# Performance work log

Hardware: AMD Instinct MI355X
Metric: run time of the kernel (lower is better)

Reference implementation:

```python
import jax, jax.numpy as jnp
import numpy as np

N = 50000      # nodes
E = 800000     # edges
D = 128        # node_feat_dim
ED = 64        # edge_feat_dim
C = 10         # num_fine_classes
BN_EPS = 1e-5


def _lin(key, fan_in, fan_out):
    k1, k2 = jax.random.split(key)
    s = 1.0 / np.sqrt(fan_in)
    W = jax.random.uniform(k1, (fan_in, fan_out), jnp.float32, -s, s)
    b = jax.random.uniform(k2, (fan_out,), jnp.float32, -s, s)
    return W, b


def setup_inputs() -> dict:
    key = jax.random.key(0)
    ks = jax.random.split(key, 16)
    nfeats = jax.random.normal(ks[0], (N, D), jnp.float32)
    efeats = jax.random.normal(ks[1], (E, ED), jnp.float32)
    src = jax.random.randint(ks[2], (E,), 0, N, jnp.int64 if jax.config.jax_enable_x64 else jnp.int32)
    dst = jax.random.randint(ks[3], (E,), 0, N, src.dtype)
    # SAGE layer 1 and 2 (E-GraphSAGE style)
    Wm1, bm1 = _lin(ks[4], D + ED, D)   # W_msg: cat(h_src, e) -> D
    Wa1, ba1 = _lin(ks[5], 2 * D, D)    # W_apply: cat(h, h_neigh) -> D
    Wm2, bm2 = _lin(ks[6], D + ED, D)
    Wa2, ba2 = _lin(ks[7], 2 * D, D)
    # coarse head: Linear(2D,32) -> ReLU -> Linear(32,2)
    Wc1, bc1 = _lin(ks[8], 2 * D, 32)
    Wc2, bc2 = _lin(ks[9], 32, 2)
    # fine head: Linear(2D,64) -> BN(64) -> ReLU -> Dropout(eval) -> Linear(64,C)
    Wf1, bf1 = _lin(ks[10], 2 * D, 64)
    bn_g = jnp.ones((64,), jnp.float32)
    bn_b = jnp.zeros((64,), jnp.float32)
    bn_m = jax.random.normal(ks[11], (64,), jnp.float32) * 0.1
    bn_v = jax.random.uniform(ks[12], (64,), jnp.float32, 0.5, 1.5)
    Wf2, bf2 = _lin(ks[13], 64, C)
    return dict(nfeats=nfeats, efeats=efeats, src=src, dst=dst,
                Wm1=Wm1, bm1=bm1, Wa1=Wa1, ba1=ba1,
                Wm2=Wm2, bm2=bm2, Wa2=Wa2, ba2=ba2,
                Wc1=Wc1, bc1=bc1, Wc2=Wc2, bc2=bc2,
                Wf1=Wf1, bf1=bf1, bn_g=bn_g, bn_b=bn_b, bn_m=bn_m, bn_v=bn_v,
                Wf2=Wf2, bf2=bf2)


def _sage_layer(h, efeats, src, dst, Wm, bm, Wa, ba):
    # per-edge message from source node + edge feature
    m = jnp.concatenate([h[src], efeats], axis=1) @ Wm + bm        # [E, D]
    # mean-aggregate messages onto destination nodes
    summed = jax.ops.segment_sum(m, dst, num_segments=N)            # [N, D]
    deg = jax.ops.segment_sum(jnp.ones((E, 1), h.dtype), dst, num_segments=N)
    h_neigh = summed / jnp.maximum(deg, 1.0)
    return jax.nn.leaky_relu(jnp.concatenate([h, h_neigh], axis=1) @ Wa + ba, 0.01)


def reference(nfeats, efeats, src, dst,
              Wm1, bm1, Wa1, ba1, Wm2, bm2, Wa2, ba2,
              Wc1, bc1, Wc2, bc2,
              Wf1, bf1, bn_g, bn_b, bn_m, bn_v, Wf2, bf2):
    h = _sage_layer(nfeats, efeats, src, dst, Wm1, bm1, Wa1, ba1)
    h = _sage_layer(h, efeats, src, dst, Wm2, bm2, Wa2, ba2)  # dropout is identity in eval
    pair = jnp.concatenate([h[src], h[dst]], axis=1)           # [E, 2D]
    coarse = jax.nn.relu(pair @ Wc1 + bc1) @ Wc2 + bc2         # [E, 2]
    x = pair @ Wf1 + bf1
    x = bn_g * (x - bn_m) * jax.lax.rsqrt(bn_v + BN_EPS) + bn_b  # eval-mode BatchNorm1d
    fine = jax.nn.relu(x) @ Wf2 + bf2                            # [E, C]
    return coarse, fine
```

## Files before the change

kernel.cpp:

```cpp
#include <hip/hip_runtime.h>

#define N_NODES 50000
#define N_EDGES 800000
#define SCAN_NBLK 196

typedef unsigned int uint;
typedef unsigned short ushort;
typedef __attribute__((ext_vector_type(4))) float f32x4;
typedef __attribute__((ext_vector_type(2))) float f32x2;
typedef __attribute__((ext_vector_type(8))) short s16x8;
typedef __attribute__((ext_vector_type(4))) uint u32x4;

__device__ __forceinline__ float bf2f(uint lo16) { return __uint_as_float(lo16 << 16); }
__device__ __forceinline__ ushort f2bf(float f) {
    uint u = __float_as_uint(f);
    u = u + 0x7fffu + ((u >> 16) & 1u);
    return (ushort)(u >> 16);
}
__device__ __forceinline__ bool is_bf16(const uint* tag) { return *tag != 0x3F800000u; }
__device__ __forceinline__ float ldf(const void* p, long i, bool bf) {
    return bf ? bf2f(((const ushort*)p)[i]) : ((const float*)p)[i];
}

__global__ __launch_bounds__(256) void k_prep(
    const void* Wm1, const void* Wa1, const void* Wm2, const void* Wa2,
    const void* Wc1, const void* Wf1,
    ushort* wA1, ushort* wB1, ushort* wa1, ushort* wA2, ushort* wB2, ushort* wa2, ushort* wPF,
    const void* bc1, const void* wc2, const void* bc2,
    const void* bf1, const void* g, const void* bb, const void* m, const void* v,
    const void* wf2, const void* bf2,
    const void* bm1, const void* ba1, const void* bm2, const void* ba2,
    float* __restrict__ pp, int* __restrict__ cur, const uint* __restrict__ tag)
{
    const bool bf = is_bf16(tag);
    int gidx = blockIdx.x * 256 + threadIdx.x;
    if (gidx < N_NODES) cur[gidx] = 0;

    if (blockIdx.x == 544) {
        int t = threadIdx.x; const int T = 256;
        for (int i = t; i < 32; i += T) pp[i] = ldf(bc1, i, bf);
        for (int i = t; i < 64; i += T) pp[32 + i] = ldf(wc2, i, bf);
        for (int i = t; i < 2;  i += T) pp[96 + i] = ldf(bc2, i, bf);
        for (int i = t; i < 64; i += T) {
            float s_ = ldf(g, i, bf) * rsqrtf(ldf(v, i, bf) + 1e-5f);
            pp[98 + i]  = s_;
            pp[162 + i] = (ldf(bf1, i, bf) - ldf(m, i, bf)) * s_ + ldf(bb, i, bf);
        }
        for (int i = t; i < 640; i += T) pp[226 + i] = ldf(wf2, i, bf);
        for (int i = t; i < 10;  i += T) pp[866 + i] = ldf(bf2, i, bf);
        for (int i = t; i < 128; i += T) {
            pp[876 + i]  = ldf(bm1, i, bf);
            pp[1004 + i] = ldf(ba1, i, bf);
            pp[1132 + i] = ldf(bm2, i, bf);
            pp[1260 + i] = ldf(ba2, i, bf);
        }
        return;
    }

    int idx = gidx;
#define SEG(SZ, Wp, LDW, RO, KC, Dp) \
    if (idx < (SZ)) { int n_ = idx / (KC), k_ = idx & ((KC) - 1); \
        (Dp)[n_ * (KC) + k_] = f2bf(ldf((Wp), (long)((RO) + k_) * (LDW) + n_, bf)); return; } \
    idx -= (SZ);
    SEG(16384, Wm1, 128, 0,   128, wA1)
    SEG(8192,  Wm1, 128, 128, 64,  wB1)
    SEG(32768, Wa1, 128, 0,   256, wa1)
    SEG(16384, Wm2, 128, 0,   128, wA2)
    SEG(8192,  Wm2, 128, 128, 64,  wB2)
    SEG(32768, Wa2, 128, 0,   256, wa2)
    SEG(4096,  Wc1, 32,  0,   128, wPF)
    SEG(4096,  Wc1, 32,  128, 128, wPF + 32 * 128)
    SEG(8192,  Wf1, 64,  0,   128, wPF + 64 * 128)
    SEG(8192,  Wf1, 64,  128, 128, wPF + 128 * 128)
#undef SEG
}

__global__ void k_count(const int* __restrict__ dst, int* __restrict__ cnt) {
    int e = blockIdx.x * 256 + threadIdx.x;
    if (e < N_EDGES) atomicAdd(&cnt[dst[e]], 1);
}

__global__ __launch_bounds__(256) void k_scan1(const int* __restrict__ cnt,
                                               int* __restrict__ rs, int* __restrict__ bsum)
{
    __shared__ int sh[256];
    int tid = threadIdx.x;
    int n = blockIdx.x * 256 + tid;
    int c = (n < N_NODES) ? cnt[n] : 0;
    sh[tid] = c;
    __syncthreads();
    #pragma unroll
    for (int off = 1; off < 256; off <<= 1) {
        int v = (tid >= off) ? sh[tid - off] : 0;
        __syncthreads();
        sh[tid] += v;
        __syncthreads();
    }
    if (n < N_NODES) rs[n] = sh[tid] - c;
    if (tid == 255) bsum[blockIdx.x] = sh[255];
}

__global__ __launch_bounds__(256) void k_scan23(const int* __restrict__ bsum,
                                                int* __restrict__ rs, int* __restrict__ cur)
{
    __shared__ int sh[256];
    int tid = threadIdx.x;
    int v = (tid < SCAN_NBLK) ? bsum[tid] : 0;
    sh[tid] = v;
    __syncthreads();
    #pragma unroll
    for (int off = 1; off < 256; off <<= 1) {
        int u = (tid >= off) ? sh[tid - off] : 0;
        __syncthreads();
        sh[tid] += u;
        __syncthreads();
    }
    int boff = (blockIdx.x == 0) ? 0 : sh[blockIdx.x - 1];
    int n = blockIdx.x * 256 + tid;
    if (n < N_NODES) {
        int r = rs[n] + boff;
        rs[n] = r;
        cur[n] = r;
    }
    if (blockIdx.x == 0 && tid == 0) rs[N_NODES] = sh[SCAN_NBLK - 1];
}

__global__ void k_fill(const int* __restrict__ dst, const int* __restrict__ src,
                       int* __restrict__ cur, int* __restrict__ eidx, int* __restrict__ ssrc) {
    int e = blockIdx.x * 256 + threadIdx.x;
    if (e < N_EDGES) {
        int p = atomicAdd(&cur[dst[e]], 1);
        eidx[p] = e;
        ssrc[p] = src[e];
    }
}

__global__ __launch_bounds__(256) void k_sef(
    const void* __restrict__ ef, const int* __restrict__ rs, const int* __restrict__ eix,
    float* __restrict__ sef, const uint* __restrict__ tag)
{
    bool bf = is_bf16(tag);
    int n = blockIdx.x * 4 + (threadIdx.x >> 6);
    if (n >= N_NODES) return;
    int lane = threadIdx.x & 63;
    int s0 = rs[n], s1 = rs[n + 1];
    if (bf) {
        int g = lane >> 3, l = lane & 7;
        const ushort* efp = (const ushort*)ef;
        float acc[8] = {};
        for (int base = s0; base < s1; base += 64) {
            int cnt = s1 - base; if (cnt > 64) cnt = 64;
            int pre = (base + lane < s1) ? eix[base + lane] : 0;
            int T = (cnt + 7) >> 3;
            for (int t = 0; t < T; t += 2) {
                int j0 = g + t * 8;
                int j1 = j0 + 8;
                long e0 = __shfl(pre, j0, 64);
                long e1 = __shfl(pre, j1 & 63, 64);
                if (j0 < cnt) {
                    u32x4 u0 = *(const u32x4*)(efp + e0 * 64 + l * 8);
                    #pragma unroll
                    for (int q = 0; q < 4; q++) {
                        acc[2 * q]     += bf2f(u0[q] & 0xffffu);
                        acc[2 * q + 1] += bf2f(u0[q] >> 16);
                    }
                }
                if (j1 < cnt) {
                    u32x4 u1 = *(const u32x4*)(efp + e1 * 64 + l * 8);
                    #pragma unroll
                    for (int q = 0; q < 4; q++) {
                        acc[2 * q]     += bf2f(u1[q] & 0xffffu);
                        acc[2 * q + 1] += bf2f(u1[q] >> 16);
                    }
                }
            }
        }
        #pragma unroll
        for (int m = 0; m < 8; m++) {
            acc[m] += __shfl_xor(acc[m], 8, 64);
            acc[m] += __shfl_xor(acc[m], 16, 64);
            acc[m] += __shfl_xor(acc[m], 32, 64);
        }
        if (g == 0) {
            *(f32x4*)&sef[(long)n * 64 + l * 8]     = f32x4{acc[0], acc[1], acc[2], acc[3]};
            *(f32x4*)&sef[(long)n * 64 + l * 8 + 4] = f32x4{acc[4], acc[5], acc[6], acc[7]};
        }
    } else {
        int g = lane >> 4, l = lane & 15;
        const float* efp = (const float*)ef;
        f32x4 acc = {0.f, 0.f, 0.f, 0.f};
        for (int base = s0; base < s1; base += 64) {
            int cnt = s1 - base; if (cnt > 64) cnt = 64;
            int pre = (base + lane < s1) ? eix[base + lane] : 0;
            int T = (cnt + 3) >> 2;
            for (int t = 0; t < T; t += 2) {
                int j0 = g + t * 4;
                int j1 = j0 + 4;
                long e0 = __shfl(pre, j0, 64);
                long e1 = __shfl(pre, j1 & 63, 64);
                if (j0 < cnt) acc += *(const f32x4*)(efp + e0 * 64 + l * 4);
                if (j1 < cnt) acc += *(const f32x4*)(efp + e1 * 64 + l * 4);
            }
        }
        #pragma unroll
        for (int m = 0; m < 4; m++) {
            acc[m] += __shfl_xor(acc[m], 16, 64);
            acc[m] += __shfl_xor(acc[m], 32, 64);
        }
        if (g == 0) *(f32x4*)&sef[(long)n * 64 + l * 4] = acc;
    }
}

template<int K1, int NOUT, int EPI>
__device__ __forceinline__ void gemm_body(ushort* xs,
    const void* __restrict__ X1, int dt1,
    const ushort* __restrict__ Wt,
    void* __restrict__ Y, int M, bool bf, int mblk)
{
    constexpr int K = K1;
    constexpr int KT = K / 32;
    constexpr int NT = NOUT / 16;
    constexpr int PITCH = K + 8;
    constexpr int KP = K / 2;
    const int m0 = mblk * 64;
    const int tid = threadIdx.x;

    for (int idx = tid; idx < 64 * KP; idx += 256) {
        int r = idx / KP, kp = idx - r * KP;
        int row = m0 + r;
        uint val = 0u;
        if (row < M) {
            long base = (long)row * K1 + kp * 2;
            bool f32src = (dt1 == 2) || (dt1 == 1 && !bf);
            if (f32src) {
                const float* fp = (const float*)X1;
                val = (uint)f2bf(fp[base]) | ((uint)f2bf(fp[base + 1]) << 16);
            } else {
                val = ((const uint*)X1)[base >> 1];
            }
        }
        *(uint*)&xs[r * PITCH + kp * 2] = val;
    }
    __syncthreads();

    const int lane = tid & 63, wid = tid >> 6;
    const int l16 = lane & 15, lh = lane >> 4;

    s16x8 afr[KT];
    const ushort* xrow = &xs[(wid * 16 + l16) * PITCH + lh * 8];
    #pragma unroll
    for (int ks = 0; ks < KT; ks++) afr[ks] = *(const s16x8*)(xrow + ks * 32);

    f32x4 acc[NT] = {};
    #pragma unroll
    for (int nt = 0; nt < NT; nt++) {
        const ushort* wrow = &Wt[(long)(nt * 16 + l16) * K + lh * 8];
        #pragma unroll
        for (int ks = 0; ks < KT; ks++) {
            s16x8 bfr = *(const s16x8*)(wrow + ks * 32);
            acc[nt] = __builtin_amdgcn_mfma_f32_16x16x32_bf16(afr[ks], bfr, acc[nt], 0, 0, 0);
        }
    }

    #pragma unroll
    for (int nt = 0; nt < NT; nt++) {
        int col = nt * 16 + l16;
        #pragma unroll
        for (int r = 0; r < 4; r++) {
            int row = m0 + wid * 16 + lh * 4 + r;
            if (row < M) {
                float v = acc[nt][r];
                if (EPI == 2) ((float*)Y)[(long)row * NOUT + col] = v;
                else          ((ushort*)Y)[(long)row * NOUT + col] = f2bf(v);
            }
        }
    }
}

__global__ __launch_bounds__(256) void k_fat3(
    const void* __restrict__ XA, int dtA, const ushort* __restrict__ wA, ushort* __restrict__ A,
    const float* __restrict__ sef,
    const ushort* __restrict__ wB1, float* __restrict__ SB1,
    const ushort* __restrict__ wB2, float* __restrict__ SB2,
    int nA, const uint* __restrict__ tag)
{
    __shared__ ushort xs[64 * 136];
    bool bf = is_bf16(tag);
    int b = blockIdx.x;
    if (b < nA)
        gemm_body<128, 128, 0>(xs, XA, dtA, wA, A, N_NODES, bf, b);
    else if (b < 2 * nA)
        gemm_body<64, 128, 2>(xs, sef, 2, wB1, SB1, N_NODES, bf, b - nA);
    else
        gemm_body<64, 128, 2>(xs, sef, 2, wB2, SB2, N_NODES, bf, b - 2 * nA);
}

__global__ __launch_bounds__(256) void k_agg(
    const ushort* __restrict__ A, const float* __restrict__ SB,
    const int* __restrict__ rs, const int* __restrict__ ssrc,
    const float* __restrict__ bm, ushort* __restrict__ hn)
{
    int n = blockIdx.x * 4 + (threadIdx.x >> 6);
    if (n >= N_NODES) return;
    int lane = threadIdx.x & 63;
    int g = lane >> 4, l = lane & 15;
    int s0 = rs[n], s1 = rs[n + 1];
    float acc[8] = {};
    for (int base = s0; base < s1; base += 64) {
        int cnt = s1 - base; if (cnt > 64) cnt = 64;
        int pre = (base + lane < s1) ? ssrc[base + lane] : 0;
        int T = (cnt + 3) >> 2;
        for (int t = 0; t < T; t += 4) {
            int j0 = g + t * 4;
            int j1 = j0 + 4, j2 = j0 + 8, j3 = j0 + 12;
            long i0 = __shfl(pre, j0, 64);
            long i1 = __shfl(pre, j1 & 63, 64);
            long i2 = __shfl(pre, j2 & 63, 64);
            long i3 = __shfl(pre, j3 & 63, 64);
            if (j0 < cnt) {
                u32x4 u = *(const u32x4*)&A[i0 * 128 + l * 8];
                #pragma unroll
                for (int q = 0; q < 4; q++) {
                    acc[2 * q]     += bf2f(u[q] & 0xffffu);
                    acc[2 * q + 1] += bf2f(u[q] >> 16);
                }
            }
            if (j1 < cnt) {
                u32x4 u = *(const u32x4*)&A[i1 * 128 + l * 8];
                #pragma unroll
                for (int q = 0; q < 4; q++) {
                    acc[2 * q]     += bf2f(u[q] & 0xffffu);
                    acc[2 * q + 1] += bf2f(u[q] >> 16);
                }
            }
            if (j2 < cnt) {
                u32x4 u = *(const u32x4*)&A[i2 * 128 + l * 8];
                #pragma unroll
                for (int q = 0; q < 4; q++) {
                    acc[2 * q]     += bf2f(u[q] & 0xffffu);
                    acc[2 * q + 1] += bf2f(u[q] >> 16);
                }
            }
            if (j3 < cnt) {
                u32x4 u = *(const u32x4*)&A[i3 * 128 + l * 8];
                #pragma unroll
                for (int q = 0; q < 4; q++) {
                    acc[2 * q]     += bf2f(u[q] & 0xffffu);
                    acc[2 * q + 1] += bf2f(u[q] >> 16);
                }
            }
        }
    }
    #pragma unroll
    for (int m = 0; m < 8; m++) {
        acc[m] += __shfl_xor(acc[m], 16, 64);
        acc[m] += __shfl_xor(acc[m], 32, 64);
    }
    if (g == 0) {
        int deg = s1 - s0;
        u32x4 ov = {0u, 0u, 0u, 0u};
        if (deg > 0) {
            float inv = 1.f / (float)deg;
            f32x4 sb0 = *(const f32x4*)&SB[(long)n * 128 + l * 8];
            f32x4 sb1 = *(const f32x4*)&SB[(long)n * 128 + l * 8 + 4];
            float h[8];
            #pragma unroll
            for (int m = 0; m < 8; m++) {
                float sbv = (m < 4) ? sb0[m] : sb1[m - 4];
                h[m] = (acc[m] + sbv) * inv + bm[l * 8 + m];
            }
            #pragma unroll
            for (int q = 0; q < 4; q++)
                ov[q] = (uint)f2bf(h[2 * q]) | ((uint)f2bf(h[2 * q + 1]) << 16);
        }
        *(u32x4*)&hn[(long)n * 128 + l * 8] = ov;
    }
}

template<int MODE>
__global__ __launch_bounds__(256) void k_apply(
    const void* __restrict__ X1, int dt1, const ushort* __restrict__ hn,
    const ushort* __restrict__ Wt, const float* __restrict__ bias,
    ushort* __restrict__ Hout,
    const ushort* __restrict__ Wt2, ushort* __restrict__ Y2a, ushort* __restrict__ Y2b,
    const uint* __restrict__ tag)
{
    constexpr int PITCH = 264;
    constexpr int NT2 = MODE ? 12 : 8;
    __shared__ ushort xs[64 * PITCH];
    __shared__ ushort ys[64 * 136];
    const bool bf = is_bf16(tag);
    const int m0 = blockIdx.x * 64;
    const int tid = threadIdx.x;
    const int lane = tid & 63, wid = tid >> 6;

    for (int idx = tid; idx < 64 * 128; idx += 256) {
        int r = idx >> 7, kp = idx & 127;
        int row = m0 + r;
        uint val = 0u;
        if (row < N_NODES) {
            if (kp < 64) {
                long base = (long)row * 128 + kp * 2;
                if (dt1 == 1 && !bf) {
                    const float* fp = (const float*)X1;
                    val = (uint)f2bf(fp[base]) | ((uint)f2bf(fp[base + 1]) << 16);
                } else {
                    val = ((const uint*)X1)[base >> 1];
                }
            } else {
                val = ((const uint*)hn)[((long)row * 128 + (kp - 64) * 2) >> 1];
            }
        }
        *(uint*)&xs[r * PITCH + kp * 2] = val;
    }
    __syncthreads();

    const int l16 = lane & 15, lh = lane >> 4;

    s16x8 afr[8];
    const ushort* xrow = &xs[(wid * 16 + l16) * PITCH + lh * 8];
    #pragma unroll
    for (int ks = 0; ks < 8; ks++) afr[ks] = *(const s16x8*)(xrow + ks * 32);

    f32x4 acc[8] = {};
    #pragma unroll
    for (int nt = 0; nt < 8; nt++) {
        const ushort* wrow = &Wt[(long)(nt * 16 + l16) * 256 + lh * 8];
        #pragma unroll
        for (int ks = 0; ks < 8; ks++) {
            s16x8 bfr = *(const s16x8*)(wrow + ks * 32);
            acc[nt] = __builtin_amdgcn_mfma_f32_16x16x32_bf16(afr[ks], bfr, acc[nt], 0, 0, 0);
        }
    }

    #pragma unroll
    for (int nt = 0; nt < 8; nt++) {
        int col = nt * 16 + l16;
        float bv = bias[col];
        #pragma unroll
        for (int r = 0; r < 4; r++) {
            int rl = wid * 16 + lh * 4 + r;
            int row = m0 + rl;
            float v = acc[nt][r] + bv;
            v = v > 0.f ? v : 0.01f * v;
            ushort hv = f2bf(v);
            ys[rl * 136 + col] = hv;
            if (MODE == 0 && row < N_NODES)
                Hout[(long)row * 128 + col] = hv;
        }
    }
    __syncthreads();

    s16x8 af2[4];
    const ushort* yrow = &ys[(wid * 16 + l16) * 136 + lh * 8];
    #pragma unroll
    for (int ks = 0; ks < 4; ks++) af2[ks] = *(const s16x8*)(yrow + ks * 32);

    f32x4 ac2[NT2] = {};
    #pragma unroll
    for (int nt = 0; nt < NT2; nt++) {
        const ushort* wrow = &Wt2[(long)(nt * 16 + l16) * 128 + lh * 8];
        #pragma unroll
        for (int ks = 0; ks < 4; ks++) {
            s16x8 bfr = *(const s16x8*)(wrow + ks * 32);
            ac2[nt] = __builtin_amdgcn_mfma_f32_16x16x32_bf16(af2[ks], bfr, ac2[nt], 0, 0, 0);
        }
    }
    #pragma unroll
    for (int nt = 0; nt < NT2; nt++) {
        int col = nt * 16 + l16;
        ushort* T; int c2;
        if (MODE == 0) {
            T = Y2a; c2 = col;
        } else {
            if (col < 64) { T = (col < 32) ? Y2a : Y2b; c2 = col & 31; }
            else if (col < 128) { T = Y2a; c2 = col - 32; }
            else                { T = Y2b; c2 = col - 96; }
        }
        #pragma unroll
        for (int r = 0; r < 4; r++) {
            int row = m0 + wid * 16 + lh * 4 + r;
            if (row < N_NODES)
                T[(long)row * 128 + c2] = f2bf(ac2[nt][r]);
        }
    }
}

__global__ __launch_bounds__(256) void k_head(
    const ushort* __restrict__ PFs, const ushort* __restrict__ PFd,
    const int* __restrict__ src, const int* __restrict__ dst,
    const float* __restrict__ pp, void* __restrict__ out, const uint* __restrict__ tag)
{
    __shared__ float sp[876];
    for (int i = threadIdx.x; i < 876; i += 256) sp[i] = pp[i];
    __syncthreads();
    const float* bc1 = sp;        const float* wc2 = sp + 32;  const float* bc2 = sp + 96;
    const float* sbn = sp + 98;   const float* tbn = sp + 162;
    const float* wf2 = sp + 226;  const float* bf2 = sp + 866;
    bool bf = is_bf16(tag);
    int e = blockIdx.x * 256 + threadIdx.x;
    if (e >= N_EDGES) return;
    int s = src[e], d = dst[e];
    const ushort* ps = PFs + (long)s * 128;
    const ushort* pd = PFd + (long)d * 128;

    float c0 = bc2[0], c1 = bc2[1];
    #pragma unroll
    for (int jb = 0; jb < 32; jb += 8) {
        u32x4 ua = *(const u32x4*)(ps + jb);
        u32x4 ub = *(const u32x4*)(pd + jb);
        #pragma unroll
        for (int q = 0; q < 4; q++) {
            int j = jb + q * 2;
            float p0 = bf2f(ua[q] & 0xffffu) + bf2f(ub[q] & 0xffffu) + bc1[j];
            float p1 = bf2f(ua[q] >> 16)     + bf2f(ub[q] >> 16)     + bc1[j + 1];
            p0 = fmaxf(p0, 0.f);
            p1 = fmaxf(p1, 0.f);
            c0 += p0 * wc2[j * 2 + 0] + p1 * wc2[j * 2 + 2];
            c1 += p0 * wc2[j * 2 + 1] + p1 * wc2[j * 2 + 3];
        }
    }

    float fa[10];
    #pragma unroll
    for (int j = 0; j < 10; j++) fa[j] = bf2[j];
    #pragma unroll
    for (int db = 0; db < 64; db += 8) {
        u32x4 ua = *(const u32x4*)(ps + 32 + db);
        u32x4 ub = *(const u32x4*)(pd + 32 + db);
        #pragma unroll
        for (int q = 0; q < 4; q++) {
            int dd = db + q * 2;
            float x0 = (bf2f(ua[q] & 0xffffu) + bf2f(ub[q] & 0xffffu)) * sbn[dd] + tbn[dd];
            float x1 = (bf2f(ua[q] >> 16)     + bf2f(ub[q] >> 16))     * sbn[dd + 1] + tbn[dd + 1];
            x0 = fmaxf(x0, 0.f);
            x1 = fmaxf(x1, 0.f);
            #pragma unroll
            for (int j = 0; j < 10; j++)
                fa[j] += x0 * wf2[dd * 10 + j] + x1 * wf2[(dd + 1) * 10 + j];
        }
    }

    if (bf) {
        uint* oc = (uint*)out;
        oc[e] = (uint)f2bf(c0) | ((uint)f2bf(c1) << 16);
        uint* of = (uint*)((ushort*)out + 2L * N_EDGES + 10L * e);
        #pragma unroll
        for (int j = 0; j < 5; j++)
            of[j] = (uint)f2bf(fa[2 * j]) | ((uint)f2bf(fa[2 * j + 1]) << 16);
    } else {
        float* o = (float*)out;
        *(f32x2*)&o[2L * e] = f32x2{c0, c1};
        float* of = o + 2L * N_EDGES + 10L * e;
        #pragma unroll
        for (int j = 0; j < 5; j++)
            *(f32x2*)&of[2 * j] = f32x2{fa[2 * j], fa[2 * j + 1]};
    }
}

extern "C" void kernel_launch(void* const* d_in, const int* in_sizes, int n_in,
                              void* d_out, int out_size, void* d_ws, size_t ws_size,
                              hipStream_t stream)
{
    (void)in_sizes; (void)n_in; (void)out_size; (void)ws_size;
    const void* nf  = d_in[0];
    const void* ef  = d_in[1];
    const int* src  = (const int*)d_in[2];
    const int* dst  = (const int*)d_in[3];
    const void* Wm1 = d_in[4];  const void* bm1 = d_in[5];
    const void* Wa1 = d_in[6];  const void* ba1 = d_in[7];
    const void* Wm2 = d_in[8];  const void* bm2 = d_in[9];
    const void* Wa2 = d_in[10]; const void* ba2 = d_in[11];
    const void* Wc1 = d_in[12]; const void* bc1 = d_in[13];
    const void* Wc2 = d_in[14]; const void* bc2 = d_in[15];
    const void* Wf1 = d_in[16]; const void* bf1 = d_in[17];
    const void* bng = d_in[18]; const void* bnb = d_in[19];
    const void* bnm = d_in[20]; const void* bnv = d_in[21];
    const void* Wf2 = d_in[22]; const void* bf2 = d_in[23];
    const uint* tag = (const uint*)d_in[18];

    char* w = (char*)d_ws;
    size_t o = 0;
    auto alloc = [&](size_t b) -> char* { char* p = w + o; o += (b + 255) & ~(size_t)255; return p; };
    ushort* wA1 = (ushort*)alloc(128 * 128 * 2);
    ushort* wB1 = (ushort*)alloc(128 * 64 * 2);
    ushort* wa1 = (ushort*)alloc(128 * 256 * 2);
    ushort* wA2 = (ushort*)alloc(128 * 128 * 2);
    ushort* wB2 = (ushort*)alloc(128 * 64 * 2);
    ushort* wa2 = (ushort*)alloc(128 * 256 * 2);
    ushort* wPF = (ushort*)alloc(192 * 128 * 2);
    float*  pp  = (float*)alloc(1388 * 4);
    int*    rs  = (int*)alloc((N_NODES + 1) * 4);
    int*    cur = (int*)alloc(N_NODES * 4);
    int*    bsum = (int*)alloc(SCAN_NBLK * 4);
    int*    eix = (int*)alloc((size_t)N_EDGES * 4);
    int*    ssr = (int*)alloc((size_t)N_EDGES * 4);
    float*  sef = (float*)alloc((size_t)N_NODES * 64 * 4);
    float*  SB1 = (float*)alloc((size_t)N_NODES * 128 * 4);
    float*  SB2 = (float*)alloc((size_t)N_NODES * 128 * 4);
    ushort* A   = (ushort*)alloc((size_t)N_NODES * 128 * 2);
    ushort* hn  = (ushort*)alloc((size_t)N_NODES * 128 * 2);
    ushort* h1  = (ushort*)alloc((size_t)N_NODES * 128 * 2);
    ushort* PFs = (ushort*)alloc((size_t)N_NODES * 128 * 2);
    ushort* PFd = (ushort*)alloc((size_t)N_NODES * 128 * 2);

    const int GB_N = (N_NODES + 63) / 64;
    const int EB   = N_EDGES / 256;
    const int NB4  = (N_NODES + 3) / 4;

    k_prep<<<545, 256, 0, stream>>>(Wm1, Wa1, Wm2, Wa2, Wc1, Wf1,
                                    wA1, wB1, wa1, wA2, wB2, wa2, wPF,
                                    bc1, Wc2, bc2, bf1, bng, bnb, bnm, bnv, Wf2, bf2,
                                    bm1, ba1, bm2, ba2, pp, cur, tag);
    k_count<<<EB, 256, 0, stream>>>(dst, cur);
    k_scan1<<<SCAN_NBLK, 256, 0, stream>>>(cur, rs, bsum);
    k_scan23<<<SCAN_NBLK, 256, 0, stream>>>(bsum, rs, cur);
    k_fill<<<EB, 256, 0, stream>>>(dst, src, cur, eix, ssr);
    k_sef<<<NB4, 256, 0, stream>>>(ef, rs, eix, sef, tag);

    k_fat3<<<3 * GB_N, 256, 0, stream>>>(nf, 1, wA1, A, sef, wB1, SB1, wB2, SB2, GB_N, tag);

    k_agg<<<NB4, 256, 0, stream>>>(A, SB1, rs, ssr, pp + 876, hn);
    k_apply<0><<<GB_N, 256, 0, stream>>>(nf, 1, hn, wa1, pp + 1004, h1,
                                         wA2, A, nullptr, tag);

    k_agg<<<NB4, 256, 0, stream>>>(A, SB2, rs, ssr, pp + 1132, hn);
    k_apply<1><<<GB_N, 256, 0, stream>>>(h1, 0, hn, wa2, pp + 1260, nullptr,
                                         wPF, PFs, PFd, tag);

    k_head<<<EB, 256, 0, stream>>>(PFs, PFd, src, dst, pp, d_out, tag);
}
```

Before: 480.9 us.

## Aggregate raw node and edge features before message GEMM, fuse into mega kernel

Linearity of mean aggregation is used to sum raw source-node features and edge features per destination node first, then a single fused kernel applies the concatenated message weight, divides by degree, adds the bias and runs the apply GEMM (plus the head projection in layer 2). This removes the per-node precomputed A/SB buffers, the separate k_fat3 GEMM launch and the separate aggregation-apply steps, cutting launches and intermediate traffic. The trade-off is that layer 2 gathers h1 rows into a 192-wide fp32 buffer and the mega kernel does a K=192 GEMM per block, and summation order changes numerics slightly.

```diff
diff --git a/kernel.cpp b/kernel.cpp
--- a/kernel.cpp
+++ b/kernel.cpp
@@ -10,6 +10,7 @@
 typedef __attribute__((ext_vector_type(2))) float f32x2;
 typedef __attribute__((ext_vector_type(8))) short s16x8;
 typedef __attribute__((ext_vector_type(4))) uint u32x4;
+typedef __attribute__((ext_vector_type(2))) uint u32x2;
 
 __device__ __forceinline__ float bf2f(uint lo16) { return __uint_as_float(lo16 << 16); }
 __device__ __forceinline__ ushort f2bf(float f) {
@@ -17,6 +18,9 @@
     u = u + 0x7fffu + ((u >> 16) & 1u);
     return (ushort)(u >> 16);
 }
+__device__ __forceinline__ uint pack2(float a, float b) {
+    return (uint)f2bf(a) | ((uint)f2bf(b) << 16);
+}
 __device__ __forceinline__ bool is_bf16(const uint* tag) { return *tag != 0x3F800000u; }
 __device__ __forceinline__ float ldf(const void* p, long i, bool bf) {
     return bf ? bf2f(((const ushort*)p)[i]) : ((const float*)p)[i];
@@ -25,7 +29,7 @@
 __global__ __launch_bounds__(256) void k_prep(
     const void* Wm1, const void* Wa1, const void* Wm2, const void* Wa2,
     const void* Wc1, const void* Wf1,
-    ushort* wA1, ushort* wB1, ushort* wa1, ushort* wA2, ushort* wB2, ushort* wa2, ushort* wPF,
+    ushort* wM1, ushort* wa1, ushort* wM2, ushort* wa2, ushort* wPF,
     const void* bc1, const void* wc2, const void* bc2,
     const void* bf1, const void* g, const void* bb, const void* m, const void* v,
     const void* wf2, const void* bf2,
@@ -59,15 +63,13 @@
 
     int idx = gidx;
 #define SEG(SZ, Wp, LDW, RO, KC, Dp) \
-    if (idx < (SZ)) { int n_ = idx / (KC), k_ = idx & ((KC) - 1); \
+    if (idx < (SZ)) { int n_ = idx / (KC), k_ = idx % (KC); \
         (Dp)[n_ * (KC) + k_] = f2bf(ldf((Wp), (long)((RO) + k_) * (LDW) + n_, bf)); return; } \
     idx -= (SZ);
-    SEG(16384, Wm1, 128, 0,   128, wA1)
-    SEG(8192,  Wm1, 128, 128, 64,  wB1)
-    SEG(32768, Wa1, 128, 0,   256, wa1)
-    SEG(16384, Wm2, 128, 0,   128, wA2)
-    SEG(8192,  Wm2, 128, 128, 64,  wB2)
-    SEG(32768, Wa2, 128, 0,   256, wa2)
+    SEG(24576, Wm1, 128, 0, 192, wM1)
+    SEG(32768, Wa1, 128, 0, 256, wa1)
+    SEG(24576, Wm2, 128, 0, 192, wM2)
+    SEG(32768, Wa2, 128, 0, 256, wa2)
     SEG(4096,  Wc1, 32,  0,   128, wPF)
     SEG(4096,  Wc1, 32,  128, 128, wPF + 32 * 128)
     SEG(8192,  Wf1, 64,  0,   128, wPF + 64 * 128)
@@ -135,170 +137,97 @@
     }
 }
 
-__global__ __launch_bounds__(256) void k_sef(
-    const void* __restrict__ ef, const int* __restrict__ rs, const int* __restrict__ eix,
-    float* __restrict__ sef, const uint* __restrict__ tag)
+__global__ __launch_bounds__(256) void k_gather1(
+    const void* __restrict__ nf, const void* __restrict__ ef,
+    const int* __restrict__ rs, const int* __restrict__ eix, const int* __restrict__ ssrc,
+    float* __restrict__ S, const uint* __restrict__ tag)
 {
     bool bf = is_bf16(tag);
     int n = blockIdx.x * 4 + (threadIdx.x >> 6);
     if (n >= N_NODES) return;
     int lane = threadIdx.x & 63;
+    int g = lane >> 4, l = lane & 15;
     int s0 = rs[n], s1 = rs[n + 1];
-    if (bf) {
-        int g = lane >> 3, l = lane & 7;
-        const ushort* efp = (const ushort*)ef;
-        float acc[8] = {};
-        for (int base = s0; base < s1; base += 64) {
-            int cnt = s1 - base; if (cnt > 64) cnt = 64;
-            int pre = (base + lane < s1) ? eix[base + lane] : 0;
-            int T = (cnt + 7) >> 3;
-            for (int t = 0; t < T; t += 2) {
-                int j0 = g + t * 8;
-                int j1 = j0 + 8;
-                long e0 = __shfl(pre, j0, 64);
-                long e1 = __shfl(pre, j1 & 63, 64);
+    float anf[8] = {};
+    float aef[4] = {};
+    for (int base = s0; base < s1; base += 64) {
+        int cnt = s1 - base; if (cnt > 64) cnt = 64;
+        int ps = (base + lane < s1) ? ssrc[base + lane] : 0;
+        int pe = (base + lane < s1) ? eix[base + lane] : 0;
+        int T = (cnt + 3) >> 2;
+        for (int t = 0; t < T; t += 2) {
+            int j0 = g + t * 4;
+            int j1 = j0 + 4;
+            long is0 = __shfl(ps, j0, 64);
+            long ie0 = __shfl(pe, j0, 64);
+            long is1 = __shfl(ps, j1 & 63, 64);
+            long ie1 = __shfl(pe, j1 & 63, 64);
+            if (bf) {
+                const ushort* nfp = (const ushort*)nf;
+                const ushort* efp = (const ushort*)ef;
                 if (j0 < cnt) {
-                    u32x4 u0 = *(const u32x4*)(efp + e0 * 64 + l * 8);
+                    u32x4 a = *(const u32x4*)(nfp + is0 * 128 + l * 8);
+                    u32x2 b = *(const u32x2*)(efp + ie0 * 64 + l * 4);
                     #pragma unroll
                     for (int q = 0; q < 4; q++) {
-                        acc[2 * q]     += bf2f(u0[q] & 0xffffu);
-                        acc[2 * q + 1] += bf2f(u0[q] >> 16);
+                        anf[2 * q]     += bf2f(a[q] & 0xffffu);
+                        anf[2 * q + 1] += bf2f(a[q] >> 16);
                     }
+                    aef[0] += bf2f(b[0] & 0xffffu); aef[1] += bf2f(b[0] >> 16);
+                    aef[2] += bf2f(b[1] & 0xffffu); aef[3] += bf2f(b[1] >> 16);
                 }
                 if (j1 < cnt) {
-                    u32x4 u1 = *(const u32x4*)(efp + e1 * 64 + l * 8);
+                    u32x4 a = *(const u32x4*)(nfp + is1 * 128 + l * 8);
+                    u32x2 b = *(const u32x2*)(efp + ie1 * 64 + l * 4);
                     #pragma unroll
                     for (int q = 0; q < 4; q++) {
-                        acc[2 * q]     += bf2f(u1[q] & 0xffffu);
-                        acc[2 * q + 1] += bf2f(u1[q] >> 16);
+                        anf[2 * q]     += bf2f(a[q] & 0xffffu);
+                        anf[2 * q + 1] += bf2f(a[q] >> 16);
                     }
+                    aef[0] += bf2f(b[0] & 0xffffu); aef[1] += bf2f(b[0] >> 16);
+                    aef[2] += bf2f(b[1] & 0xffffu); aef[3] += bf2f(b[1] >> 16);
                 }
-            }
-        }
-        #pragma unroll
-        for (int m = 0; m < 8; m++) {
-            acc[m] += __shfl_xor(acc[m], 8, 64);
-            acc[m] += __shfl_xor(acc[m], 16, 64);
-            acc[m] += __shfl_xor(acc[m], 32, 64);
-        }
-        if (g == 0) {
-            *(f32x4*)&sef[(long)n * 64 + l * 8]     = f32x4{acc[0], acc[1], acc[2], acc[3]};
-            *(f32x4*)&sef[(long)n * 64 + l * 8 + 4] = f32x4{acc[4], acc[5], acc[6], acc[7]};
-        }
-    } else {
-        int g = lane >> 4, l = lane & 15;
-        const float* efp = (const float*)ef;
-        f32x4 acc = {0.f, 0.f, 0.f, 0.f};
-        for (int base = s0; base < s1; base += 64) {
-            int cnt = s1 - base; if (cnt > 64) cnt = 64;
-            int pre = (base + lane < s1) ? eix[base + lane] : 0;
-            int T = (cnt + 3) >> 2;
-            for (int t = 0; t < T; t += 2) {
-                int j0 = g + t * 4;
-                int j1 = j0 + 4;
-                long e0 = __shfl(pre, j0, 64);
-                long e1 = __shfl(pre, j1 & 63, 64);
-                if (j0 < cnt) acc += *(const f32x4*)(efp + e0 * 64 + l * 4);
-                if (j1 < cnt) acc += *(const f32x4*)(efp + e1 * 64 + l * 4);
-            }
-        }
-        #pragma unroll
-        for (int m = 0; m < 4; m++) {
-            acc[m] += __shfl_xor(acc[m], 16, 64);
-            acc[m] += __shfl_xor(acc[m], 32, 64);
-        }
-        if (g == 0) *(f32x4*)&sef[(long)n * 64 + l * 4] = acc;
-    }
-}
-
-template<int K1, int NOUT, int EPI>
-__device__ __forceinline__ void gemm_body(ushort* xs,
-    const void* __restrict__ X1, int dt1,
-    const ushort* __restrict__ Wt,
-    void* __restrict__ Y, int M, bool bf, int mblk)
-{
-    constexpr int K = K1;
-    constexpr int KT = K / 32;
-    constexpr int NT = NOUT / 16;
-    constexpr int PITCH = K + 8;
-    constexpr int KP = K / 2;
-    const int m0 = mblk * 64;
-    const int tid = threadIdx.x;
-
-    for (int idx = tid; idx < 64 * KP; idx += 256) {
-        int r = idx / KP, kp = idx - r * KP;
-        int row = m0 + r;
-        uint val = 0u;
-        if (row < M) {
-            long base = (long)row * K1 + kp * 2;
-            bool f32src = (dt1 == 2) || (dt1 == 1 && !bf);
-            if (f32src) {
-                const float* fp = (const float*)X1;
-                val = (uint)f2bf(fp[base]) | ((uint)f2bf(fp[base + 1]) << 16);
             } else {
-                val = ((const uint*)X1)[base >> 1];
-            }
-        }
-        *(uint*)&xs[r * PITCH + kp * 2] = val;
-    }
-    __syncthreads();
-
-    const int lane = tid & 63, wid = tid >> 6;
-    const int l16 = lane & 15, lh = lane >> 4;
-
-    s16x8 afr[KT];
-    const ushort* xrow = &xs[(wid * 16 + l16) * PITCH + lh * 8];
-    #pragma unroll
-    for (int ks = 0; ks < KT; ks++) afr[ks] = *(const s16x8*)(xrow + ks * 32);
-
-    f32x4 acc[NT] = {};
-    #pragma unroll
-    for (int nt = 0; nt < NT; nt++) {
-        const ushort* wrow = &Wt[(long)(nt * 16 + l16) * K + lh * 8];
-        #pragma unroll
-        for (int ks = 0; ks < KT; ks++) {
-            s16x8 bfr = *(const s16x8*)(wrow + ks * 32);
-            acc[nt] = __builtin_amdgcn_mfma_f32_16x16x32_bf16(afr[ks], bfr, acc[nt], 0, 0, 0);
-        }
-    }
-
-    #pragma unroll
-    for (int nt = 0; nt < NT; nt++) {
-        int col = nt * 16 + l16;
-        #pragma unroll
-        for (int r = 0; r < 4; r++) {
-            int row = m0 + wid * 16 + lh * 4 + r;
-            if (row < M) {
-                float v = acc[nt][r];
-                if (EPI == 2) ((float*)Y)[(long)row * NOUT + col] = v;
-                else          ((ushort*)Y)[(long)row * NOUT + col] = f2bf(v);
-            }
-        }
-    }
-}
-
-__global__ __launch_bounds__(256) void k_fat3(
-    const void* __restrict__ XA, int dtA, const ushort* __restrict__ wA, ushort* __restrict__ A,
-    const float* __restrict__ sef,
-    const ushort* __restrict__ wB1, float* __restrict__ SB1,
-    const ushort* __restrict__ wB2, float* __restrict__ SB2,
-    int nA, const uint* __restrict__ tag)
-{
-    __shared__ ushort xs[64 * 136];
-    bool bf = is_bf16(tag);
-    int b = blockIdx.x;
-    if (b < nA)
-        gemm_body<128, 128, 0>(xs, XA, dtA, wA, A, N_NODES, bf, b);
-    else if (b < 2 * nA)
-        gemm_body<64, 128, 2>(xs, sef, 2, wB1, SB1, N_NODES, bf, b - nA);
-    else
-        gemm_body<64, 128, 2>(xs, sef, 2, wB2, SB2, N_NODES, bf, b - 2 * nA);
-}
-
-__global__ __launch_bounds__(256) void k_agg(
-    const ushort* __restrict__ A, const float* __restrict__ SB,
-    const int* __restrict__ rs, const int* __restrict__ ssrc,
-    const float* __restrict__ bm, ushort* __restrict__ hn)
+                const float* nfp = (const float*)nf;
+                const float* efp = (const float*)ef;
+                if (j0 < cnt) {
+                    f32x4 a0 = *(const f32x4*)(nfp + is0 * 128 + l * 8);
+                    f32x4 a1 = *(const f32x4*)(nfp + is0 * 128 + l * 8 + 4);
+                    f32x4 b  = *(const f32x4*)(efp + ie0 * 64 + l * 4);
+                    #pragma unroll
+                    for (int q = 0; q < 4; q++) { anf[q] += a0[q]; anf[4 + q] += a1[q]; aef[q] += b[q]; }
+                }
+                if (j1 < cnt) {
+                    f32x4 a0 = *(const f32x4*)(nfp + is1 * 128 + l * 8);
+                    f32x4 a1 = *(const f32x4*)(nfp + is1 * 128 + l * 8 + 4);
+                    f32x4 b  = *(const f32x4*)(efp + ie1 * 64 + l * 4);
+                    #pragma unroll
+                    for (int q = 0; q < 4; q++) { anf[q] += a0[q]; anf[4 + q] += a1[q]; aef[q] += b[q]; }
+                }
+            }
+        }
+    }
+    #pragma unroll
+    for (int m = 0; m < 8; m++) {
+        anf[m] += __shfl_xor(anf[m], 16, 64);
+        anf[m] += __shfl_xor(anf[m], 32, 64);
+    }
+    #pragma unroll
+    for (int m = 0; m < 4; m++) {
+        aef[m] += __shfl_xor(aef[m], 16, 64);
+        aef[m] += __shfl_xor(aef[m], 32, 64);
+    }
+    if (g == 0) {
+        float* Sr = S + (long)n * 192;
+        *(f32x4*)&Sr[l * 8]     = f32x4{anf[0], anf[1], anf[2], anf[3]};
+        *(f32x4*)&Sr[l * 8 + 4] = f32x4{anf[4], anf[5], anf[6], anf[7]};
+        *(f32x4*)&Sr[128 + l * 4] = f32x4{aef[0], aef[1], aef[2], aef[3]};
+    }
+}
+
+__global__ __launch_bounds__(256) void k_gather2(
+    const ushort* __restrict__ H, const int* __restrict__ rs, const int* __restrict__ ssrc,
+    float* __restrict__ S)
 {
     int n = blockIdx.x * 4 + (threadIdx.x >> 6);
     if (n >= N_NODES) return;
@@ -308,46 +237,34 @@
     float acc[8] = {};
     for (int base = s0; base < s1; base += 64) {
         int cnt = s1 - base; if (cnt > 64) cnt = 64;
-        int pre = (base + lane < s1) ? ssrc[base + lane] : 0;
+        int ps = (base + lane < s1) ? ssrc[base + lane] : 0;
         int T = (cnt + 3) >> 2;
         for (int t = 0; t < T; t += 4) {
             int j0 = g + t * 4;
             int j1 = j0 + 4, j2 = j0 + 8, j3 = j0 + 12;
-            long i0 = __shfl(pre, j0, 64);
-            long i1 = __shfl(pre, j1 & 63, 64);
-            long i2 = __shfl(pre, j2 & 63, 64);
-            long i3 = __shfl(pre, j3 & 63, 64);
+            long i0 = __shfl(ps, j0, 64);
+            long i1 = __shfl(ps, j1 & 63, 64);
+            long i2 = __shfl(ps, j2 & 63, 64);
+            long i3 = __shfl(ps, j3 & 63, 64);
             if (j0 < cnt) {
-                u32x4 u = *(const u32x4*)&A[i0 * 128 + l * 8];
+                u32x4 u = *(const u32x4*)&H[i0 * 128 + l * 8];
                 #pragma unroll
-                for (int q = 0; q < 4; q++) {
-                    acc[2 * q]     += bf2f(u[q] & 0xffffu);
-                    acc[2 * q + 1] += bf2f(u[q] >> 16);
-                }
+                for (int q = 0; q < 4; q++) { acc[2*q] += bf2f(u[q] & 0xffffu); acc[2*q+1] += bf2f(u[q] >> 16); }
             }
             if (j1 < cnt) {
-                u32x4 u = *(const u32x4*)&A[i1 * 128 + l * 8];
+                u32x4 u = *(const u32x4*)&H[i1 * 128 + l * 8];
                 #pragma unroll
-                for (int q = 0; q < 4; q++) {
-                    acc[2 * q]     += bf2f(u[q] & 0xffffu);
-                    acc[2 * q + 1] += bf2f(u[q] >> 16);
-                }
+                for (int q = 0; q < 4; q++) { acc[2*q] += bf2f(u[q] & 0xffffu); acc[2*q+1] += bf2f(u[q] >> 16); }
             }
             if (j2 < cnt) {
-                u32x4 u = *(const u32x4*)&A[i2 * 128 + l * 8];
+                u32x4 u = *(const u32x4*)&H[i2 * 128 + l * 8];
                 #pragma unroll
-                for (int q = 0; q < 4; q++) {
-                    acc[2 * q]     += bf2f(u[q] & 0xffffu);
-                    acc[2 * q + 1] += bf2f(u[q] >> 16);
-                }
+                for (int q = 0; q < 4; q++) { acc[2*q] += bf2f(u[q] & 0xffffu); acc[2*q+1] += bf2f(u[q] >> 16); }
             }
             if (j3 < cnt) {
-                u32x4 u = *(const u32x4*)&A[i3 * 128 + l * 8];
+                u32x4 u = *(const u32x4*)&H[i3 * 128 + l * 8];
                 #pragma unroll
-                for (int q = 0; q < 4; q++) {
-                    acc[2 * q]     += bf2f(u[q] & 0xffffu);
-                    acc[2 * q + 1] += bf2f(u[q] >> 16);
-                }
+                for (int q = 0; q < 4; q++) { acc[2*q] += bf2f(u[q] & 0xffffu); acc[2*q+1] += bf2f(u[q] >> 16); }
             }
         }
     }
@@ -357,131 +274,160 @@
         acc[m] += __shfl_xor(acc[m], 32, 64);
     }
     if (g == 0) {
-        int deg = s1 - s0;
-        u32x4 ov = {0u, 0u, 0u, 0u};
-        if (deg > 0) {
-            float inv = 1.f / (float)deg;
-            f32x4 sb0 = *(const f32x4*)&SB[(long)n * 128 + l * 8];
-            f32x4 sb1 = *(const f32x4*)&SB[(long)n * 128 + l * 8 + 4];
-            float h[8];
-            #pragma unroll
-            for (int m = 0; m < 8; m++) {
-                float sbv = (m < 4) ? sb0[m] : sb1[m - 4];
-                h[m] = (acc[m] + sbv) * inv + bm[l * 8 + m];
-            }
-            #pragma unroll
-            for (int q = 0; q < 4; q++)
-                ov[q] = (uint)f2bf(h[2 * q]) | ((uint)f2bf(h[2 * q + 1]) << 16);
-        }
-        *(u32x4*)&hn[(long)n * 128 + l * 8] = ov;
+        float* Sr = S + (long)n * 192;
+        *(f32x4*)&Sr[l * 8]     = f32x4{acc[0], acc[1], acc[2], acc[3]};
+        *(f32x4*)&Sr[l * 8 + 4] = f32x4{acc[4], acc[5], acc[6], acc[7]};
     }
 }
 
 template<int MODE>
-__global__ __launch_bounds__(256) void k_apply(
-    const void* __restrict__ X1, int dt1, const ushort* __restrict__ hn,
-    const ushort* __restrict__ Wt, const float* __restrict__ bias,
+__global__ __launch_bounds__(256) void k_mega(
+    const float* __restrict__ S, const void* __restrict__ X,
+    const int* __restrict__ rs,
+    const ushort* __restrict__ wM, const float* __restrict__ bm,
+    const ushort* __restrict__ wa, const float* __restrict__ ba,
     ushort* __restrict__ Hout,
-    const ushort* __restrict__ Wt2, ushort* __restrict__ Y2a, ushort* __restrict__ Y2b,
+    const ushort* __restrict__ wPF, ushort* __restrict__ PFs, ushort* __restrict__ PFd,
     const uint* __restrict__ tag)
 {
     constexpr int PITCH = 264;
-    constexpr int NT2 = MODE ? 12 : 8;
     __shared__ ushort xs[64 * PITCH];
     __shared__ ushort ys[64 * 136];
+    __shared__ int sdeg[64];
     const bool bf = is_bf16(tag);
     const int m0 = blockIdx.x * 64;
     const int tid = threadIdx.x;
     const int lane = tid & 63, wid = tid >> 6;
-
-    for (int idx = tid; idx < 64 * 128; idx += 256) {
-        int r = idx >> 7, kp = idx & 127;
+    const int l16 = lane & 15, lh = lane >> 4;
+
+    for (int idx = tid; idx < 64 * 48; idx += 256) {
+        int r = idx / 48, kq = idx % 48;
         int row = m0 + r;
-        uint val = 0u;
+        u32x2 val = {0u, 0u};
         if (row < N_NODES) {
-            if (kp < 64) {
-                long base = (long)row * 128 + kp * 2;
-                if (dt1 == 1 && !bf) {
-                    const float* fp = (const float*)X1;
-                    val = (uint)f2bf(fp[base]) | ((uint)f2bf(fp[base + 1]) << 16);
-                } else {
-                    val = ((const uint*)X1)[base >> 1];
-                }
+            f32x4 s4 = *(const f32x4*)&S[(long)row * 192 + kq * 4];
+            val[0] = pack2(s4[0], s4[1]);
+            val[1] = pack2(s4[2], s4[3]);
+        }
+        *(u32x2*)&xs[r * PITCH + kq * 4] = val;
+    }
+    if (tid < 64) {
+        int n = m0 + tid;
+        sdeg[tid] = (n < N_NODES) ? rs[n + 1] - rs[n] : 0;
+    }
+    __syncthreads();
+
+    {
+        s16x8 afr[6];
+        const ushort* xrow = &xs[(wid * 16 + l16) * PITCH + lh * 8];
+        #pragma unroll
+        for (int ks = 0; ks < 6; ks++) afr[ks] = *(const s16x8*)(xrow + ks * 32);
+        f32x4 acc[8] = {};
+        #pragma unroll
+        for (int nt = 0; nt < 8; nt++) {
+            const ushort* wrow = &wM[(long)(nt * 16 + l16) * 192 + lh * 8];
+            #pragma unroll
+            for (int ks = 0; ks < 6; ks++) {
+                s16x8 bfr = *(const s16x8*)(wrow + ks * 32);
+                acc[nt] = __builtin_amdgcn_mfma_f32_16x16x32_bf16(afr[ks], bfr, acc[nt], 0, 0, 0);
+            }
+        }
+        __syncthreads();
+
+        #pragma unroll
+        for (int nt = 0; nt < 8; nt++) {
+            int col = nt * 16 + l16;
+            float bmv = bm[col];
+            #pragma unroll
+            for (int r = 0; r < 4; r++) {
+                int rl = wid * 16 + lh * 4 + r;
+                int dg = sdeg[rl];
+                float inv = dg > 0 ? 1.f / (float)dg : 0.f;
+                float hv = dg > 0 ? acc[nt][r] * inv + bmv : 0.f;
+                xs[rl * PITCH + 128 + col] = f2bf(hv);
+            }
+        }
+    }
+
+    for (int idx = tid; idx < 64 * 32; idx += 256) {
+        int r = idx >> 5, kq = idx & 31;
+        int row = m0 + r;
+        u32x2 val = {0u, 0u};
+        if (row < N_NODES) {
+            if (MODE == 0 && !bf) {
+                const float* fp = (const float*)X + (long)row * 128 + kq * 4;
+                val[0] = pack2(fp[0], fp[1]);
+                val[1] = pack2(fp[2], fp[3]);
             } else {
-                val = ((const uint*)hn)[((long)row * 128 + (kp - 64) * 2) >> 1];
-            }
-        }
-        *(uint*)&xs[r * PITCH + kp * 2] = val;
+                val = ((const u32x2*)X)[(long)row * 32 + kq];
+            }
+        }
+        *(u32x2*)&xs[r * PITCH + kq * 4] = val;
     }
     __syncthreads();
 
-    const int l16 = lane & 15, lh = lane >> 4;
-
-    s16x8 afr[8];
-    const ushort* xrow = &xs[(wid * 16 + l16) * PITCH + lh * 8];
-    #pragma unroll
-    for (int ks = 0; ks < 8; ks++) afr[ks] = *(const s16x8*)(xrow + ks * 32);
-
-    f32x4 acc[8] = {};
-    #pragma unroll
-    for (int nt = 0; nt < 8; nt++) {
-        const ushort* wrow = &Wt[(long)(nt * 16 + l16) * 256 + lh * 8];
-        #pragma unroll
-        for (int ks = 0; ks < 8; ks++) {
-            s16x8 bfr = *(const s16x8*)(wrow + ks * 32);
-            acc[nt] = __builtin_amdgcn_mfma_f32_16x16x32_bf16(afr[ks], bfr, acc[nt], 0, 0, 0);
-        }
-    }
-
-    #pragma unroll
-    for (int nt = 0; nt < 8; nt++) {
-        int col = nt * 16 + l16;
-        float bv = bias[col];
-        #pragma unroll
-        for (int r = 0; r < 4; r++) {
-            int rl = wid * 16 + lh * 4 + r;
-            int row = m0 + rl;
-            float v = acc[nt][r] + bv;
-            v = v > 0.f ? v : 0.01f * v;
-            ushort hv = f2bf(v);
-            ys[rl * 136 + col] = hv;
-            if (MODE == 0 && row < N_NODES)
-                Hout[(long)row * 128 + col] = hv;
-        }
-    }
-    __syncthreads();
-
-    s16x8 af2[4];
-    const ushort* yrow = &ys[(wid * 16 + l16) * 136 + lh * 8];
-    #pragma unroll
-    for (int ks = 0; ks < 4; ks++) af2[ks] = *(const s16x8*)(yrow + ks * 32);
-
-    f32x4 ac2[NT2] = {};
-    #pragma unroll
-    for (int nt = 0; nt < NT2; nt++) {
-        const ushort* wrow = &Wt2[(long)(nt * 16 + l16) * 128 + lh * 8];
-        #pragma unroll
-        for (int ks = 0; ks < 4; ks++) {
-            s16x8 bfr = *(const s16x8*)(wrow + ks * 32);
-            ac2[nt] = __builtin_amdgcn_mfma_f32_16x16x32_bf16(af2[ks], bfr, ac2[nt], 0, 0, 0);
-        }
-    }
-    #pragma unroll
-    for (int nt = 0; nt < NT2; nt++) {
-        int col = nt * 16 + l16;
-        ushort* T; int c2;
-        if (MODE == 0) {
-            T = Y2a; c2 = col;
-        } else {
-            if (col < 64) { T = (col < 32) ? Y2a : Y2b; c2 = col & 31; }
-            else if (col < 128) { T = Y2a; c2 = col - 32; }
-            else                { T = Y2b; c2 = col - 96; }
-        }
-        #pragma unroll
-        for (int r = 0; r < 4; r++) {
-            int row = m0 + wid * 16 + lh * 4 + r;
-            if (row < N_NODES)
-                T[(long)row * 128 + c2] = f2bf(ac2[nt][r]);
+    {
+        s16x8 afr[8];
+        const ushort* xrow = &xs[(wid * 16 + l16) * PITCH + lh * 8];
+        #pragma unroll
+        for (int ks = 0; ks < 8; ks++) afr[ks] = *(const s16x8*)(xrow + ks * 32);
+        f32x4 acc[8] = {};
+        #pragma unroll
+        for (int nt = 0; nt < 8; nt++) {
+            const ushort* wrow = &wa[(long)(nt * 16 + l16) * 256 + lh * 8];
+            #pragma unroll
+            for (int ks = 0; ks < 8; ks++) {
+                s16x8 bfr = *(const s16x8*)(wrow + ks * 32);
+                acc[nt] = __builtin_amdgcn_mfma_f32_16x16x32_bf16(afr[ks], bfr, acc[nt], 0, 0, 0);
+            }
+        }
+        #pragma unroll
+        for (int nt = 0; nt < 8; nt++) {
+            int col = nt * 16 + l16;
+            float bv = ba[col];
+            #pragma unroll
+            for (int r = 0; r < 4; r++) {
+                int rl = wid * 16 + lh * 4 + r;
+                int row = m0 + rl;
+                float v = acc[nt][r] + bv;
+                v = v > 0.f ? v : 0.01f * v;
+                ushort hv = f2bf(v);
+                ys[rl * 136 + col] = hv;
+                if (MODE == 0 && row < N_NODES)
+                    Hout[(long)row * 128 + col] = hv;
+            }
+        }
+    }
+
+    if (MODE == 1) {
+        __syncthreads();
+        s16x8 af3[4];
+        const ushort* yrow = &ys[(wid * 16 + l16) * 136 + lh * 8];
+        #pragma unroll
+        for (int ks = 0; ks < 4; ks++) af3[ks] = *(const s16x8*)(yrow + ks * 32);
+        f32x4 ac3[12] = {};
+        #pragma unroll
+        for (int nt = 0; nt < 12; nt++) {
+            const ushort* wrow = &wPF[(long)(nt * 16 + l16) * 128 + lh * 8];
+            #pragma unroll
+            for (int ks = 0; ks < 4; ks++) {
+                s16x8 bfr = *(const s16x8*)(wrow + ks * 32);
+                ac3[nt] = __builtin_amdgcn_mfma_f32_16x16x32_bf16(af3[ks], bfr, ac3[nt], 0, 0, 0);
+            }
+        }
+        #pragma unroll
+        for (int nt = 0; nt < 12; nt++) {
+            int col = nt * 16 + l16;
+            ushort* T; int c2;
+            if (col < 64) { T = (col < 32) ? PFs : PFd; c2 = col & 31; }
+            else if (col < 128) { T = PFs; c2 = col - 32; }
+            else                { T = PFd; c2 = col - 96; }
+            #pragma unroll
+            for (int r = 0; r < 4; r++) {
+                int row = m0 + wid * 16 + lh * 4 + r;
+                if (row < N_NODES)
+                    T[(long)row * 128 + c2] = f2bf(ac3[nt][r]);
+            }
         }
     }
 }
@@ -543,11 +489,11 @@
 
     if (bf) {
         uint* oc = (uint*)out;
-        oc[e] = (uint)f2bf(c0) | ((uint)f2bf(c1) << 16);
+        oc[e] = pack2(c0, c1);
         uint* of = (uint*)((ushort*)out + 2L * N_EDGES + 10L * e);
         #pragma unroll
         for (int j = 0; j < 5; j++)
-            of[j] = (uint)f2bf(fa[2 * j]) | ((uint)f2bf(fa[2 * j + 1]) << 16);
+            of[j] = pack2(fa[2 * j], fa[2 * j + 1]);
     } else {
         float* o = (float*)out;
         *(f32x2*)&o[2L * e] = f32x2{c0, c1};
@@ -582,11 +528,9 @@
     char* w = (char*)d_ws;
     size_t o = 0;
     auto alloc = [&](size_t b) -> char* { char* p = w + o; o += (b + 255) & ~(size_t)255; return p; };
-    ushort* wA1 = (ushort*)alloc(128 * 128 * 2);
-    ushort* wB1 = (ushort*)alloc(128 * 64 * 2);
+    ushort* wM1 = (ushort*)alloc(128 * 192 * 2);
     ushort* wa1 = (ushort*)alloc(128 * 256 * 2);
-    ushort* wA2 = (ushort*)alloc(128 * 128 * 2);
-    ushort* wB2 = (ushort*)alloc(128 * 64 * 2);
+    ushort* wM2 = (ushort*)alloc(128 * 192 * 2);
     ushort* wa2 = (ushort*)alloc(128 * 256 * 2);
     ushort* wPF = (ushort*)alloc(192 * 128 * 2);
     float*  pp  = (float*)alloc(1388 * 4);
@@ -595,11 +539,7 @@
     int*    bsum = (int*)alloc(SCAN_NBLK * 4);
     int*    eix = (int*)alloc((size_t)N_EDGES * 4);
     int*    ssr = (int*)alloc((size_t)N_EDGES * 4);
-    float*  sef = (float*)alloc((size_t)N_NODES * 64 * 4);
-    float*  SB1 = (float*)alloc((size_t)N_NODES * 128 * 4);
-    float*  SB2 = (float*)alloc((size_t)N_NODES * 128 * 4);
-    ushort* A   = (ushort*)alloc((size_t)N_NODES * 128 * 2);
-    ushort* hn  = (ushort*)alloc((size_t)N_NODES * 128 * 2);
+    float*  S   = (float*)alloc((size_t)N_NODES * 192 * 4);
     ushort* h1  = (ushort*)alloc((size_t)N_NODES * 128 * 2);
     ushort* PFs = (ushort*)alloc((size_t)N_NODES * 128 * 2);
     ushort* PFd = (ushort*)alloc((size_t)N_NODES * 128 * 2);
@@ -609,24 +549,21 @@
     const int NB4  = (N_NODES + 3) / 4;
 
     k_prep<<<545, 256, 0, stream>>>(Wm1, Wa1, Wm2, Wa2, Wc1, Wf1,
-                                    wA1, wB1, wa1, wA2, wB2, wa2, wPF,
+                                    wM1, wa1, wM2, wa2, wPF,
                                     bc1, Wc2, bc2, bf1, bng, bnb, bnm, bnv, Wf2, bf2,
                                     bm1, ba1, bm2, ba2, pp, cur, tag);
     k_count<<<EB, 256, 0, stream>>>(dst, cur);
     k_scan1<<<SCAN_NBLK, 256, 0, stream>>>(cur, rs, bsum);
     k_scan23<<<SCAN_NBLK, 256, 0, stream>>>(bsum, rs, cur);
     k_fill<<<EB, 256, 0, stream>>>(dst, src, cur, eix, ssr);
-    k_sef<<<NB4, 256, 0, stream>>>(ef, rs, eix, sef, tag);
-
-    k_fat3<<<3 * GB_N, 256, 0, stream>>>(nf, 1, wA1, A, sef, wB1, SB1, wB2, SB2, GB_N, tag);
-
-    k_agg<<<NB4, 256, 0, stream>>>(A, SB1, rs, ssr, pp + 876, hn);
-    k_apply<0><<<GB_N, 256, 0, stream>>>(nf, 1, hn, wa1, pp + 1004, h1,
-                                         wA2, A, nullptr, tag);
-
-    k_agg<<<NB4, 256, 0, stream>>>(A, SB2, rs, ssr, pp + 1132, hn);
-    k_apply<1><<<GB_N, 256, 0, stream>>>(h1, 0, hn, wa2, pp + 1260, nullptr,
-                                         wPF, PFs, PFd, tag);
+
+    k_gather1<<<NB4, 256, 0, stream>>>(nf, ef, rs, eix, ssr, S, tag);
+    k_mega<0><<<GB_N, 256, 0, stream>>>(S, nf, rs, wM1, pp + 876, wa1, pp + 1004,
+                                        h1, nullptr, nullptr, nullptr, tag);
+
+    k_gather2<<<NB4, 256, 0, stream>>>(h1, rs, ssr, S);
+    k_mega<1><<<GB_N, 256, 0, stream>>>(S, h1, rs, wM2, pp + 1132, wa2, pp + 1260,
+                                        nullptr, wPF, PFs, PFd, tag);
 
     k_head<<<EB, 256, 0, stream>>>(PFs, PFd, src, dst, pp, d_out, tag);
 }
```

Result: faster. 463.2 us (-3.7%).
